# Kernel optimization log

Measured on AMD Instinct MI355X. Metric: run time of the kernel, lower is better.

## Reference

```python
import jax, jax.numpy as jnp
import numpy as np

N_NODES = 100000


def setup_inputs() -> dict:
    key = jax.random.key(0)
    ks = jax.random.split(key, 6)
    x = jax.random.normal(ks[0], (N_NODES, 128), dtype=jnp.float32)
    edge_index = jax.random.randint(ks[1], (2, 1600000), 0, N_NODES, dtype=jnp.int32)
    W_gcn = jax.random.normal(ks[2], (128, 128), dtype=jnp.float32) * 0.05
    b_gcn = jax.random.normal(ks[3], (128,), dtype=jnp.float32) * 0.05
    W_fc = jax.random.normal(ks[4], (64, 128), dtype=jnp.float32) * 0.05
    b_fc = jax.random.normal(ks[5], (64,), dtype=jnp.float32) * 0.05
    return {"x": x, "edge_index": edge_index, "W_gcn": W_gcn, "b_gcn": b_gcn, "W_fc": W_fc, "b_fc": b_fc}


def _gcn_conv(x, edge_index, W, b):
    N = x.shape[0]
    # add self-loops (PyG GCNConv default add_self_loops=True)
    loops = jnp.arange(N, dtype=edge_index.dtype)
    row = jnp.concatenate([edge_index[0], loops])  # source
    col = jnp.concatenate([edge_index[1], loops])  # target (aggregation index)
    # symmetric normalization: deg computed at target with unit edge weights
    deg = jax.ops.segment_sum(jnp.ones_like(col, dtype=x.dtype), col, num_segments=N)
    deg_inv_sqrt = jnp.where(deg > 0, jax.lax.rsqrt(deg), 0.0)
    norm = deg_inv_sqrt[row] * deg_inv_sqrt[col]  # [E+N]
    xw = x @ W  # [N, nhid] - transform before aggregation
    msgs = norm[:, None] * xw[row]  # gather + scale, [E+N, nhid]
    out = jax.ops.segment_sum(msgs, col, num_segments=N)  # scatter-add
    return out + b


def reference(x, edge_index, W_gcn, b_gcn, W_fc, b_fc):
    h = _gcn_conv(x, edge_index, W_gcn, b_gcn)  # [N, nhid]
    return h @ W_fc.T + b_fc  # [N, nclass]
```

## Files before the change

### kernel.cpp

```cpp
#include <hip/hip_runtime.h>
#include <hip/hip_bf16.h>

typedef __hip_bfloat16 bf16;

#define N_NODES 100000
#define N_EDGES 1600000
#define F_IN    128
#define F_OUT   64
#define NBLK    391

#define NB_BKT   391
#define BKT_SH   8
#define BKT_CAP  4544
#define LBIN_CAP 32
#define EPB_A    4096


typedef __attribute__((ext_vector_type(8))) short vbf8;
typedef __attribute__((ext_vector_type(4))) float vf4;

__device__ __forceinline__ float ldf(const void* p, size_t i, bool isbf) {
    return isbf ? __bfloat162float(((const bf16*)p)[i]) : ((const float*)p)[i];
}
__device__ __forceinline__ void stf(void* p, size_t i, bool isbf, float v) {
    if (isbf) ((bf16*)p)[i] = __float2bfloat16(v);
    else      ((float*)p)[i] = v;
}
__device__ __forceinline__ unsigned short f2bfu(float f) {
    __hip_bfloat16 h = __float2bfloat16(f);
    union { __hip_bfloat16 h; unsigned short u; } c; c.h = h; return c.u;
}
__device__ __forceinline__ float bflo(unsigned int u) { return __uint_as_float(u << 16); }
__device__ __forceinline__ float bfhi(unsigned int u) { return __uint_as_float(u & 0xffff0000u); }

__global__ void k_detect(const unsigned short* __restrict__ w, int* __restrict__ flag,
                         int* __restrict__ gtail) {
    int t = threadIdx.x;
    if (gtail) {
        for (int i = t; i < NB_BKT; i += 512) gtail[i] = 0;
    }
    if (t < 64) {
        int good = 0;
#pragma unroll
        for (int q = 0; q < 2; ++q) {
            unsigned short v = w[2 * (t + 64 * q)];
            int e = (v >> 7) & 0xFF;
            if ((e >= 100 && e <= 140) || ((v & 0x7FFF) == 0)) good++;
        }
        unsigned long long m1 = __ballot(good >= 1), m2 = __ballot(good >= 2);
        if (t == 0) *flag = (__popcll(m1) + __popcll(m2) >= 96) ? 1 : 0;
    }
}

__global__ void k_weights(const int* __restrict__ flag,
                          const void* __restrict__ Wg, const void* __restrict__ bg,
                          const void* __restrict__ Wf, const void* __restrict__ bfc,
                          float* __restrict__ M, float* __restrict__ cvec,
                          bf16* __restrict__ Mhi, bf16* __restrict__ Mlo) {
    bool isbf = (*flag != 0);
    int t = blockIdx.x * blockDim.x + threadIdx.x;
    if (t >= F_IN * F_OUT) return;
    int k = t >> 6, c = t & 63;
    float s = 0.f;
    for (int j = 0; j < F_IN; ++j)
        s += ldf(Wg, k * F_IN + j, isbf) * ldf(Wf, c * F_IN + j, isbf);
    M[k * F_OUT + c] = s;
    if (Mhi) {
        int l    = (((k >> 3) & 3) << 4) | (c & 15);
        int fidx = ((((k >> 5) << 2) + (c >> 4)) * 64 + l) * 8 + (k & 7);
        bf16 h  = __float2bfloat16(s);
        Mhi[fidx] = h;
        Mlo[fidx] = __float2bfloat16(s - __bfloat162float(h));
    }
    if (k == 0) {
        float cs = ldf(bfc, c, isbf);
        for (int j = 0; j < F_IN; ++j)
            cs += ldf(bg, j, isbf) * ldf(Wf, c * F_IN + j, isbf);
        cvec[c] = cs;
    }
}


__global__ __launch_bounds__(256) void k_binA(const int* __restrict__ ei,
                                              int* __restrict__ gtail,
                                              unsigned* __restrict__ bkt) {
    __shared__ unsigned lbin[NB_BKT * LBIN_CAP];
    __shared__ int lcnt[NB_BKT];
    __shared__ int lbase[NB_BKT];
    int t = threadIdx.x;
    for (int b = t; b < NB_BKT; b += 256) lcnt[b] = 0;
    __syncthreads();
    int v0 = blockIdx.x * (EPB_A / 4);
#pragma unroll
    for (int q = 0; q < 4; ++q) {
        int vi = v0 + q * 256 + t;
        if (vi * 4 < N_EDGES) {
            int4 rv = ((const int4*)ei)[vi];
            int4 cv = ((const int4*)(ei + N_EDGES))[vi];
            int rs[4] = {rv.x, rv.y, rv.z, rv.w};
            int cs[4] = {cv.x, cv.y, cv.z, cv.w};
#pragma unroll
            for (int j = 0; j < 4; ++j) {
                int r = rs[j], c = cs[j];
                int b = c >> BKT_SH;
                unsigned val = (unsigned)r | ((unsigned)(c & ((1 << BKT_SH) - 1)) << 17);
                int p = atomicAdd(&lcnt[b], 1);
                if (p < LBIN_CAP) {
                    lbin[b * LBIN_CAP + p] = val;
                } else {
                    int gp = atomicAdd(&gtail[b], 1);
                    if (gp < BKT_CAP) bkt[(size_t)b * BKT_CAP + gp] = val;
                }
            }
        }
    }
    __syncthreads();
    for (int b = t; b < NB_BKT; b += 256) {
        int n = min(lcnt[b], LBIN_CAP);
        lbase[b] = atomicAdd(&gtail[b], n);
    }
    __syncthreads();
    int w = t >> 6, l = t & 63;
    for (int b = w; b < NB_BKT; b += 4) {
        int nB = min(lcnt[b], LBIN_CAP);
        int gp0 = lbase[b];
        for (int i = l; i < nB; i += 64) {
            int gp = gp0 + i;
            if (gp < BKT_CAP) bkt[(size_t)b * BKT_CAP + gp] = lbin[b * LBIN_CAP + i];
        }
    }
}

__global__ void k_bktscan(const int* __restrict__ gtail, int* __restrict__ bbase) {
    __shared__ int sm[512];
    int t = threadIdx.x;
    int v = (t < NB_BKT) ? min(gtail[t], BKT_CAP) : 0;
    sm[t] = v; __syncthreads();
    for (int s = 1; s < 512; s <<= 1) {
        int add = (t >= s) ? sm[t - s] : 0;
        __syncthreads();
        sm[t] += add;
        __syncthreads();
    }
    if (t < NB_BKT) bbase[t] = sm[t] - v;
}

__global__ __launch_bounds__(256) void k_build(const unsigned* __restrict__ bkt,
                                               const int* __restrict__ gtail,
                                               const int* __restrict__ bbase,
                                               int* __restrict__ ptr,
                                               int* __restrict__ cnt,
                                               float* __restrict__ dinv,
                                               int* __restrict__ srcs) {
    __shared__ int cntl[256], sm[256], fill[256];
    int b = blockIdx.x, t = threadIdx.x;
    int n = min(gtail[b], BKT_CAP);
    int base = bbase[b];
    cntl[t] = 0;
    __syncthreads();
    for (int i = t; i < n; i += 256)
        atomicAdd(&cntl[bkt[(size_t)b * BKT_CAP + i] >> 17], 1);
    __syncthreads();
    int v = cntl[t];
    sm[t] = v; __syncthreads();
    for (int s = 1; s < 256; s <<= 1) {
        int add = (t >= s) ? sm[t - s] : 0;
        __syncthreads();
        sm[t] += add;
        __syncthreads();
    }
    int excl = sm[t] - v;
    fill[t] = excl;
    int node = (b << BKT_SH) + t;
    if (node < N_NODES) {
        ptr[node]  = base + excl;
        cnt[node]  = v;
        dinv[node] = rsqrtf((float)(v + 1));
    }
    __syncthreads();
    for (int i = t; i < n; i += 256) {
        unsigned e = bkt[(size_t)b * BKT_CAP + i];
        int c = (int)(e >> 17);
        int p = atomicAdd(&fill[c], 1);
        srcs[base + p] = (int)(e & 0x1FFFF);
    }
}

__global__ __launch_bounds__(256) void k_xmz_mfma(const int* __restrict__ flag,
                                                  const void* __restrict__ x,
                                                  const bf16* __restrict__ Mhi,
                                                  const bf16* __restrict__ Mlo,
                                                  const float* __restrict__ dinv,
                                                  bf16* __restrict__ y) {
    int t = threadIdx.x;
    int w = t >> 6, lane = t & 63;
    int g = lane >> 4, cb = lane & 15;
    int r0 = blockIdx.x * 64 + w * 16;
    int rr = min(r0 + cb, N_NODES - 1);
    bool isbf = (*flag != 0);
    const vbf8* Bh = (const vbf8*)Mhi;
    const vbf8* Bl = (const vbf8*)Mlo;
    vf4 acc0 = {0.f,0.f,0.f,0.f}, acc1 = {0.f,0.f,0.f,0.f};
    vf4 acc2 = {0.f,0.f,0.f,0.f}, acc3 = {0.f,0.f,0.f,0.f};

    if (isbf) {
        const vbf8* X8 = (const vbf8*)x;
#pragma unroll
        for (int kk = 0; kk < 4; ++kk) {
            vbf8 a = X8[(size_t)rr * 16 + kk * 4 + g];
            int bb = kk * 256 + lane;
            acc0 = __builtin_amdgcn_mfma_f32_16x16x32_bf16(a, Bh[bb      ], acc0, 0, 0, 0);
            acc0 = __builtin_amdgcn_mfma_f32_16x16x32_bf16(a, Bl[bb      ], acc0, 0, 0, 0);
            acc1 = __builtin_amdgcn_mfma_f32_16x16x32_bf16(a, Bh[bb +  64], acc1, 0, 0, 0);
            acc1 = __builtin_amdgcn_mfma_f32_16x16x32_bf16(a, Bl[bb +  64], acc1, 0, 0, 0);
            acc2 = __builtin_amdgcn_mfma_f32_16x16x32_bf16(a, Bh[bb + 128], acc2, 0, 0, 0);
            acc2 = __builtin_amdgcn_mfma_f32_16x16x32_bf16(a, Bl[bb + 128], acc2, 0, 0, 0);
            acc3 = __builtin_amdgcn_mfma_f32_16x16x32_bf16(a, Bh[bb + 192], acc3, 0, 0, 0);
            acc3 = __builtin_amdgcn_mfma_f32_16x16x32_bf16(a, Bl[bb + 192], acc3, 0, 0, 0);
        }
    } else {
        const float4* X4 = (const float4*)x;
#pragma unroll
        for (int kk = 0; kk < 4; ++kk) {
            float4 v0 = X4[(size_t)rr * 32 + kk * 8 + g * 2];
            float4 v1 = X4[(size_t)rr * 32 + kk * 8 + g * 2 + 1];
            vbf8 ah, al;
            {
                float fv[8] = {v0.x, v0.y, v0.z, v0.w, v1.x, v1.y, v1.z, v1.w};
#pragma unroll
                for (int i = 0; i < 8; ++i) {
                    unsigned short hu = f2bfu(fv[i]);
                    ah[i] = (short)hu;
                    al[i] = (short)f2bfu(fv[i] - __uint_as_float((unsigned)hu << 16));
                }
            }
            int bb = kk * 256 + lane;
            vbf8 b0h = Bh[bb      ], b0l = Bl[bb      ];
            vbf8 b1h = Bh[bb +  64], b1l = Bl[bb +  64];
            vbf8 b2h = Bh[bb + 128], b2l = Bl[bb + 128];
            vbf8 b3h = Bh[bb + 192], b3l = Bl[bb + 192];
            acc0 = __builtin_amdgcn_mfma_f32_16x16x32_bf16(ah, b0h, acc0, 0, 0, 0);
            acc0 = __builtin_amdgcn_mfma_f32_16x16x32_bf16(ah, b0l, acc0, 0, 0, 0);
            acc0 = __builtin_amdgcn_mfma_f32_16x16x32_bf16(al, b0h, acc0, 0, 0, 0);
            acc1 = __builtin_amdgcn_mfma_f32_16x16x32_bf16(ah, b1h, acc1, 0, 0, 0);
            acc1 = __builtin_amdgcn_mfma_f32_16x16x32_bf16(ah, b1l, acc1, 0, 0, 0);
            acc1 = __builtin_amdgcn_mfma_f32_16x16x32_bf16(al, b1h, acc1, 0, 0, 0);
            acc2 = __builtin_amdgcn_mfma_f32_16x16x32_bf16(ah, b2h, acc2, 0, 0, 0);
            acc2 = __builtin_amdgcn_mfma_f32_16x16x32_bf16(ah, b2l, acc2, 0, 0, 0);
            acc2 = __builtin_amdgcn_mfma_f32_16x16x32_bf16(al, b2h, acc2, 0, 0, 0);
            acc3 = __builtin_amdgcn_mfma_f32_16x16x32_bf16(ah, b3h, acc3, 0, 0, 0);
            acc3 = __builtin_amdgcn_mfma_f32_16x16x32_bf16(ah, b3l, acc3, 0, 0, 0);
            acc3 = __builtin_amdgcn_mfma_f32_16x16x32_bf16(al, b3h, acc3, 0, 0, 0);
        }
    }

    unsigned short* yb = (unsigned short*)y;
#pragma unroll
    for (int i = 0; i < 4; ++i) {
        int r = r0 + g * 4 + i;
        if (r < N_NODES) {
            float d = dinv[r];
            unsigned short* yr = yb + (size_t)r * F_OUT + cb;
            yr[0]  = f2bfu(acc0[i] * d);
            yr[16] = f2bfu(acc1[i] * d);
            yr[32] = f2bfu(acc2[i] * d);
            yr[48] = f2bfu(acc3[i] * d);
        }
    }
}

__global__ __launch_bounds__(256) void k_agg(const int* __restrict__ flag,
                                             const int* __restrict__ ptr,
                                             const int* __restrict__ cnt,
                                             const int* __restrict__ srcs,
                                             const float* __restrict__ dinv,
                                             const bf16* __restrict__ y,
                                             const float* __restrict__ cvec,
                                             void* __restrict__ out) {
    int wid  = (blockIdx.x * 256 + threadIdx.x) >> 6;
    int lane = threadIdx.x & 63;
    int g  = lane >> 3;
    int j8 = lane & 7;
    int node = wid * 8 + g;
    bool alive = node < N_NODES;
    int n = 0, start = 0;
    if (alive) { n = cnt[node]; start = ptr[node]; }
    const uint4* y4 = (const uint4*)y;

    float acc[8];
#pragma unroll
    for (int i = 0; i < 8; ++i) acc[i] = 0.f;

    for (int b = 0; __any(b < n); b += 8) {
        int s = 0;
        int idx = b + j8;
        if (idx < n) s = srcs[start + idx];
#pragma unroll
        for (int k = 0; k < 8; ++k) {
            int su = __shfl(s, (g << 3) | k, 64);
            if (b + k < n) {
                uint4 v = y4[(size_t)su * 8 + j8];
                acc[0] += bflo(v.x); acc[1] += bfhi(v.x);
                acc[2] += bflo(v.y); acc[3] += bfhi(v.y);
                acc[4] += bflo(v.z); acc[5] += bfhi(v.z);
                acc[6] += bflo(v.w); acc[7] += bfhi(v.w);
            }
        }
    }

    if (!alive) return;
    bool isbf = (*flag != 0);
    uint4 sv = y4[(size_t)node * 8 + j8];
    float dn = dinv[node];
    const float4* cv4 = (const float4*)cvec;
    float4 c0 = cv4[j8 * 2], c1 = cv4[j8 * 2 + 1];
    size_t ob = (size_t)node * F_OUT + j8 * 8;
    if (isbf) {
        ushort4 p0, p1;
        p0.x = f2bfu(dn * (acc[0] + bflo(sv.x)) + c0.x);
        p0.y = f2bfu(dn * (acc[1] + bfhi(sv.x)) + c0.y);
        p0.z = f2bfu(dn * (acc[2] + bflo(sv.y)) + c0.z);
        p0.w = f2bfu(dn * (acc[3] + bfhi(sv.y)) + c0.w);
        p1.x = f2bfu(dn * (acc[4] + bflo(sv.z)) + c1.x);
        p1.y = f2bfu(dn * (acc[5] + bfhi(sv.z)) + c1.y);
        p1.z = f2bfu(dn * (acc[6] + bflo(sv.w)) + c1.z);
        p1.w = f2bfu(dn * (acc[7] + bfhi(sv.w)) + c1.w);
        ushort4* ob4 = (ushort4*)((unsigned short*)out + ob);
        ob4[0] = p0; ob4[1] = p1;
    } else {
        float4 q0, q1;
        q0.x = dn * (acc[0] + bflo(sv.x)) + c0.x;
        q0.y = dn * (acc[1] + bfhi(sv.x)) + c0.y;
        q0.z = dn * (acc[2] + bflo(sv.y)) + c0.z;
        q0.w = dn * (acc[3] + bfhi(sv.y)) + c0.w;
        q1.x = dn * (acc[4] + bflo(sv.z)) + c1.x;
        q1.y = dn * (acc[5] + bfhi(sv.z)) + c1.y;
        q1.z = dn * (acc[6] + bflo(sv.w)) + c1.z;
        q1.w = dn * (acc[7] + bfhi(sv.w)) + c1.w;
        float4* of4 = (float4*)((float*)out + ob);
        of4[0] = q0; of4[1] = q1;
    }
}


__global__ void k_init_deg(float* __restrict__ deg) {
    int i = blockIdx.x * blockDim.x + threadIdx.x;
    if (i < N_NODES) deg[i] = 1.0f;
}
__global__ void k_deg(const int* __restrict__ col, float* __restrict__ deg) {
    int e = blockIdx.x * blockDim.x + threadIdx.x;
    if (e < N_EDGES) atomicAdd(&deg[col[e]], 1.0f);
}
__global__ void k_dinv(float* __restrict__ deg) {
    int i = blockIdx.x * blockDim.x + threadIdx.x;
    if (i < N_NODES) deg[i] = rsqrtf(deg[i]);
}
__global__ __launch_bounds__(256) void k_xm(const int* __restrict__ flag,
                                            const void* __restrict__ x,
                                            const float* __restrict__ M,
                                            void* __restrict__ z) {
    __shared__ float Ms[F_IN * F_OUT];
    int t = threadIdx.x;
    for (int i = t; i < F_IN * F_OUT; i += 256) Ms[i] = M[i];
    __syncthreads();
    bool isbf = (*flag != 0);
    int r = blockIdx.x * 4 + (t >> 6);
    int c = t & 63;
    if (r >= N_NODES) return;
    float s = 0.f;
    if (isbf) {
        const bf16* xr = (const bf16*)x + (size_t)r * F_IN;
#pragma unroll
        for (int k = 0; k < F_IN; ++k) s += __bfloat162float(xr[k]) * Ms[k * F_OUT + c];
    } else {
        const float* xr = (const float*)x + (size_t)r * F_IN;
#pragma unroll
        for (int k = 0; k < F_IN; ++k) s += xr[k] * Ms[k * F_OUT + c];
    }
    stf(z, (size_t)r * F_OUT + c, isbf, s);
}
template <int LOGF>
__global__ __launch_bounds__(256) void k_init_acc(const int* __restrict__ flag,
                                                  const float* __restrict__ dinv,
                                                  const void* __restrict__ z,
                                                  float* __restrict__ acc, int base) {
    bool isbf = (*flag != 0);
    int t = blockIdx.x * 256 + threadIdx.x;
    int i = t >> LOGF, f = t & ((1 << LOGF) - 1);
    if (i >= N_NODES) return;
    float d = dinv[i];
    acc[t] = d * d * ldf(z, (size_t)i * F_OUT + base + f, isbf);
}
template <int LOGF>
__global__ __launch_bounds__(256) void k_scatter(const int* __restrict__ flag,
                                                 const int* __restrict__ ei,
                                                 const float* __restrict__ dinv,
                                                 const void* __restrict__ z,
                                                 float* __restrict__ acc, int base) {
    bool isbf = (*flag != 0);
    long long t = (long long)blockIdx.x * 256 + threadIdx.x;
    int e = (int)(t >> LOGF), f = (int)(t & ((1 << LOGF) - 1));
    if (e >= N_EDGES) return;
    int r = ei[e], c = ei[N_EDGES + e];
    float nm = dinv[r] * dinv[c];
    float v  = nm * ldf(z, (size_t)r * F_OUT + base + f, isbf);
    atomicAdd(&acc[((size_t)c << LOGF) + f], v);
}
template <int LOGF>
__global__ __launch_bounds__(256) void k_final(const int* __restrict__ flag,
                                               const float* __restrict__ acc,
                                               const float* __restrict__ cvec,
                                               void* __restrict__ out, int base) {
    bool isbf = (*flag != 0);
    int t = blockIdx.x * 256 + threadIdx.x;
    int i = t >> LOGF, f = t & ((1 << LOGF) - 1);
    if (i >= N_NODES) return;
    stf(out, (size_t)i * F_OUT + base + f, isbf, acc[t] + cvec[base + f]);
}
template <int LOGF>
static void run_passes(const int* flag, const int* ei, const float* dinv,
                       const void* z, float* acc, const float* cvec, void* out,
                       hipStream_t stream) {
    const int fpp = 1 << LOGF;
    const long long tn = (long long)N_NODES * fpp;
    const long long te = (long long)N_EDGES * fpp;
    const int gn = (int)((tn + 255) / 256);
    const int ge = (int)((te + 255) / 256);
    for (int base = 0; base < F_OUT; base += fpp) {
        k_init_acc<LOGF><<<gn, 256, 0, stream>>>(flag, dinv, z, acc, base);
        k_scatter<LOGF><<<ge, 256, 0, stream>>>(flag, ei, dinv, z, acc, base);
        k_final<LOGF><<<gn, 256, 0, stream>>>(flag, acc, cvec, out, base);
    }
}

extern "C" void kernel_launch(void* const* d_in, const int* in_sizes, int n_in,
                              void* d_out, int out_size, void* d_ws, size_t ws_size,
                              hipStream_t stream) {
    const void* x   = d_in[0];
    const int*  ei  = (const int*)d_in[1];
    const void* Wg  = d_in[2];
    const void* bg  = d_in[3];
    const void* Wf  = d_in[4];
    const void* bfc = d_in[5];
    char* ws = (char*)d_ws;

    const size_t CSR_NEED = 20871168;
    if (ws_size >= CSR_NEED) {
        int*      flag  = (int*)(ws + 0);
        float*    dinv  = (float*)(ws + 256);
        float*    M     = (float*)(ws + 400384);
        float*    cvec  = (float*)(ws + 433152);
        int*      cnt   = (int*)(ws + 433664);
        int*      ptr   = (int*)(ws + 833664);
        int*      gtail = (int*)(ws + 1233664);
        int*      bbase = (int*)(ws + 1235264);
        int*      srcs  = (int*)(ws + 1238528);
        bf16*     y     = (bf16*)(ws + 8038400);
        unsigned* bkt   = (unsigned*)(ws + 8038400);
        bf16*     Mhi   = (bf16*)(ws + 20838400);
        bf16*     Mlo   = (bf16*)(ws + 20854784);

        k_detect<<<1, 512, 0, stream>>>((const unsigned short*)x, flag, gtail);
        k_weights<<<(F_IN * F_OUT) / 256, 256, 0, stream>>>(flag, Wg, bg, Wf, bfc, M, cvec, Mhi, Mlo);
        k_binA<<<(N_EDGES + EPB_A - 1) / EPB_A, 256, 0, stream>>>(ei, gtail, bkt);
        k_bktscan<<<1, 512, 0, stream>>>(gtail, bbase);
        k_build<<<NB_BKT, 256, 0, stream>>>(bkt, gtail, bbase, ptr, cnt, dinv, srcs);
        k_xmz_mfma<<<(N_NODES + 63) / 64, 256, 0, stream>>>(flag, x, Mhi, Mlo, dinv, y);
        k_agg<<<3125, 256, 0, stream>>>(flag, ptr, cnt, srcs, dinv, y, cvec, d_out);
    } else {
        int*   flag = (int*)(ws + 0);
        float* deg  = (float*)(ws + 256);
        float* M    = (float*)(ws + 400384);
        float* cvec = (float*)(ws + 433152);
        float* acc  = (float*)(ws + 433664);

        k_detect<<<1, 512, 0, stream>>>((const unsigned short*)x, flag, (int*)nullptr);
        k_init_deg<<<NBLK, 256, 0, stream>>>(deg);
        k_deg<<<N_EDGES / 256, 256, 0, stream>>>(ei + N_EDGES, deg);
        k_dinv<<<NBLK, 256, 0, stream>>>(deg);
        k_weights<<<(F_IN * F_OUT) / 256, 256, 0, stream>>>(flag, Wg, bg, Wf, bfc, M, cvec, (bf16*)nullptr, (bf16*)nullptr);
        k_xm<<<N_NODES / 4, 256, 0, stream>>>(flag, x, M, d_out);
        const size_t bn = 433664;
        if      (ws_size >= bn + (400000ull << 6)) run_passes<6>(flag, ei, deg, d_out, acc, cvec, d_out, stream);
        else if (ws_size >= bn + (400000ull << 5)) run_passes<5>(flag, ei, deg, d_out, acc, cvec, d_out, stream);
        else if (ws_size >= bn + (400000ull << 4)) run_passes<4>(flag, ei, deg, d_out, acc, cvec, d_out, stream);
        else if (ws_size >= bn + (400000ull << 3)) run_passes<3>(flag, ei, deg, d_out, acc, cvec, d_out, stream);
        else if (ws_size >= bn + (400000ull << 2)) run_passes<2>(flag, ei, deg, d_out, acc, cvec, d_out, stream);
        else if (ws_size >= bn + (400000ull << 1)) run_passes<1>(flag, ei, deg, d_out, acc, cvec, d_out, stream);
        else                                       run_passes<0>(flag, ei, deg, d_out, acc, cvec, d_out, stream);
    }
}
```

Measured before the change: 227.4 us.

## Fuse detect and bucket-scan kernels, widen buckets to 512 nodes

Folds the dtype detection and gtail reset into the weights kernel and drops the separate bucket-scan kernel by having each build block reduce the preceding bucket counts itself. Buckets grow to 512 nodes (196 buckets, 512-thread build blocks) with larger capacities. It also swaps the round-to-nearest hi/lo bf16 split for a truncation split. The aim is fewer kernel launches and less serialization, at the cost of redundant per-block reductions and fewer, larger build blocks.

```diff
diff --git a/kernel.cpp b/kernel.cpp
--- a/kernel.cpp
+++ b/kernel.cpp
@@ -9,10 +9,10 @@
 #define F_OUT   64
 #define NBLK    391
 
-#define NB_BKT   391
-#define BKT_SH   8
-#define BKT_CAP  4544
-#define LBIN_CAP 32
+#define NB_BKT   196
+#define BKT_SH   9
+#define BKT_CAP  8960
+#define LBIN_CAP 56
 #define EPB_A    4096
 
 
@@ -33,32 +33,32 @@
 __device__ __forceinline__ float bflo(unsigned int u) { return __uint_as_float(u << 16); }
 __device__ __forceinline__ float bfhi(unsigned int u) { return __uint_as_float(u & 0xffff0000u); }
 
-__global__ void k_detect(const unsigned short* __restrict__ w, int* __restrict__ flag,
-                         int* __restrict__ gtail) {
-    int t = threadIdx.x;
-    if (gtail) {
-        for (int i = t; i < NB_BKT; i += 512) gtail[i] = 0;
-    }
-    if (t < 64) {
-        int good = 0;
-#pragma unroll
-        for (int q = 0; q < 2; ++q) {
-            unsigned short v = w[2 * (t + 64 * q)];
-            int e = (v >> 7) & 0xFF;
-            if ((e >= 100 && e <= 140) || ((v & 0x7FFF) == 0)) good++;
-        }
-        unsigned long long m1 = __ballot(good >= 1), m2 = __ballot(good >= 2);
-        if (t == 0) *flag = (__popcll(m1) + __popcll(m2) >= 96) ? 1 : 0;
-    }
-}
-
-__global__ void k_weights(const int* __restrict__ flag,
+__global__ __launch_bounds__(256) void k_weights(const unsigned short* __restrict__ xs,
                           const void* __restrict__ Wg, const void* __restrict__ bg,
                           const void* __restrict__ Wf, const void* __restrict__ bfc,
                           float* __restrict__ M, float* __restrict__ cvec,
-                          bf16* __restrict__ Mhi, bf16* __restrict__ Mlo) {
-    bool isbf = (*flag != 0);
-    int t = blockIdx.x * blockDim.x + threadIdx.x;
+                          bf16* __restrict__ Mhi, bf16* __restrict__ Mlo,
+                          int* __restrict__ flag, int* __restrict__ gtail) {
+    __shared__ int sflag;
+    int lt = threadIdx.x;
+    if (lt < 64) {
+        int good = 0;
+#pragma unroll
+        for (int q = 0; q < 2; ++q) {
+            unsigned short v = xs[2 * (lt + 64 * q)];
+            int e = (v >> 7) & 0xFF;
+            if ((e >= 100 && e <= 140) || ((v & 0x7FFF) == 0)) good++;
+        }
+        unsigned long long m1 = __ballot(good >= 1), m2 = __ballot(good >= 2);
+        if (lt == 0) sflag = (__popcll(m1) + __popcll(m2) >= 96) ? 1 : 0;
+    }
+    __syncthreads();
+    bool isbf = (sflag != 0);
+    if (blockIdx.x == 0) {
+        if (lt == 0) *flag = sflag;
+        if (gtail && lt < NB_BKT) gtail[lt] = 0;
+    }
+    int t = blockIdx.x * 256 + lt;
     if (t >= F_IN * F_OUT) return;
     int k = t >> 6, c = t & 63;
     float s = 0.f;
@@ -131,39 +131,31 @@
     }
 }
 
-__global__ void k_bktscan(const int* __restrict__ gtail, int* __restrict__ bbase) {
-    __shared__ int sm[512];
-    int t = threadIdx.x;
-    int v = (t < NB_BKT) ? min(gtail[t], BKT_CAP) : 0;
-    sm[t] = v; __syncthreads();
-    for (int s = 1; s < 512; s <<= 1) {
-        int add = (t >= s) ? sm[t - s] : 0;
-        __syncthreads();
-        sm[t] += add;
-        __syncthreads();
-    }
-    if (t < NB_BKT) bbase[t] = sm[t] - v;
-}
-
-__global__ __launch_bounds__(256) void k_build(const unsigned* __restrict__ bkt,
+__global__ __launch_bounds__(512) void k_build(const unsigned* __restrict__ bkt,
                                                const int* __restrict__ gtail,
-                                               const int* __restrict__ bbase,
                                                int* __restrict__ ptr,
                                                int* __restrict__ cnt,
                                                float* __restrict__ dinv,
                                                int* __restrict__ srcs) {
-    __shared__ int cntl[256], sm[256], fill[256];
+    __shared__ int cntl[512], sm[512], fill[512];
     int b = blockIdx.x, t = threadIdx.x;
     int n = min(gtail[b], BKT_CAP);
-    int base = bbase[b];
+    int gv = (t < b) ? min(gtail[t], BKT_CAP) : 0;
+    sm[t] = gv; __syncthreads();
+#pragma unroll
+    for (int s = 256; s >= 1; s >>= 1) {
+        if (t < s) sm[t] += sm[t + s];
+        __syncthreads();
+    }
+    int base = sm[0];
     cntl[t] = 0;
     __syncthreads();
-    for (int i = t; i < n; i += 256)
+    for (int i = t; i < n; i += 512)
         atomicAdd(&cntl[bkt[(size_t)b * BKT_CAP + i] >> 17], 1);
     __syncthreads();
     int v = cntl[t];
     sm[t] = v; __syncthreads();
-    for (int s = 1; s < 256; s <<= 1) {
+    for (int s = 1; s < 512; s <<= 1) {
         int add = (t >= s) ? sm[t - s] : 0;
         __syncthreads();
         sm[t] += add;
@@ -178,7 +170,7 @@
         dinv[node] = rsqrtf((float)(v + 1));
     }
     __syncthreads();
-    for (int i = t; i < n; i += 256) {
+    for (int i = t; i < n; i += 512) {
         unsigned e = bkt[(size_t)b * BKT_CAP + i];
         int c = (int)(e >> 17);
         int p = atomicAdd(&fill[c], 1);
@@ -229,9 +221,10 @@
                 float fv[8] = {v0.x, v0.y, v0.z, v0.w, v1.x, v1.y, v1.z, v1.w};
 #pragma unroll
                 for (int i = 0; i < 8; ++i) {
-                    unsigned short hu = f2bfu(fv[i]);
-                    ah[i] = (short)hu;
-                    al[i] = (short)f2bfu(fv[i] - __uint_as_float((unsigned)hu << 16));
+                    unsigned bi = __float_as_uint(fv[i]);
+                    ah[i] = (short)(bi >> 16);
+                    float r = fv[i] - __uint_as_float(bi & 0xffff0000u);
+                    al[i] = (short)(__float_as_uint(r) >> 16);
                 }
             }
             int bb = kk * 256 + lane;
@@ -453,18 +446,16 @@
         int*      cnt   = (int*)(ws + 433664);
         int*      ptr   = (int*)(ws + 833664);
         int*      gtail = (int*)(ws + 1233664);
-        int*      bbase = (int*)(ws + 1235264);
         int*      srcs  = (int*)(ws + 1238528);
         bf16*     y     = (bf16*)(ws + 8038400);
         unsigned* bkt   = (unsigned*)(ws + 8038400);
         bf16*     Mhi   = (bf16*)(ws + 20838400);
         bf16*     Mlo   = (bf16*)(ws + 20854784);
 
-        k_detect<<<1, 512, 0, stream>>>((const unsigned short*)x, flag, gtail);
-        k_weights<<<(F_IN * F_OUT) / 256, 256, 0, stream>>>(flag, Wg, bg, Wf, bfc, M, cvec, Mhi, Mlo);
+        k_weights<<<(F_IN * F_OUT) / 256, 256, 0, stream>>>((const unsigned short*)x,
+                    Wg, bg, Wf, bfc, M, cvec, Mhi, Mlo, flag, gtail);
         k_binA<<<(N_EDGES + EPB_A - 1) / EPB_A, 256, 0, stream>>>(ei, gtail, bkt);
-        k_bktscan<<<1, 512, 0, stream>>>(gtail, bbase);
-        k_build<<<NB_BKT, 256, 0, stream>>>(bkt, gtail, bbase, ptr, cnt, dinv, srcs);
+        k_build<<<NB_BKT, 512, 0, stream>>>(bkt, gtail, ptr, cnt, dinv, srcs);
         k_xmz_mfma<<<(N_NODES + 63) / 64, 256, 0, stream>>>(flag, x, Mhi, Mlo, dinv, y);
         k_agg<<<3125, 256, 0, stream>>>(flag, ptr, cnt, srcs, dinv, y, cvec, d_out);
     } else {
@@ -474,11 +465,11 @@
         float* cvec = (float*)(ws + 433152);
         float* acc  = (float*)(ws + 433664);
 
-        k_detect<<<1, 512, 0, stream>>>((const unsigned short*)x, flag, (int*)nullptr);
+        k_weights<<<(F_IN * F_OUT) / 256, 256, 0, stream>>>((const unsigned short*)x,
+                    Wg, bg, Wf, bfc, M, cvec, (bf16*)nullptr, (bf16*)nullptr, flag, (int*)nullptr);
         k_init_deg<<<NBLK, 256, 0, stream>>>(deg);
         k_deg<<<N_EDGES / 256, 256, 0, stream>>>(ei + N_EDGES, deg);
         k_dinv<<<NBLK, 256, 0, stream>>>(deg);
-        k_weights<<<(F_IN * F_OUT) / 256, 256, 0, stream>>>(flag, Wg, bg, Wf, bfc, M, cvec, (bf16*)nullptr, (bf16*)nullptr);
         k_xm<<<N_NODES / 4, 256, 0, stream>>>(flag, x, M, d_out);
         const size_t bn = 433664;
         if      (ws_size >= bn + (400000ull << 6)) run_passes<6>(flag, ei, deg, d_out, acc, cvec, d_out, stream);
```

After: 214.9 us (median of 2 runs). -5.5%, faster.
